# Kernel optimization log

Measured on AMD Instinct MI355X. Metric: run time of the kernel, lower is better.

Reference implementation:

```python
import jax, jax.numpy as jnp
import numpy as np

RADIUS = 1.0
NSAMPLE = 32


def setup_inputs() -> dict:
    key = jax.random.key(0)
    k1, k2, k3, k4, k5 = jax.random.split(key, 5)
    B, Nb, M, K, C = 2, 2048, 64, 216, 32
    N = B * Nb
    # points in a 20m cube
    xyz = jax.random.uniform(k1, (N, 3), dtype=jnp.float32) * 20.0
    xyz_batch_cnt = jnp.array([Nb, Nb], dtype=jnp.int32)
    # rois: [x,y,z,dx,dy,dz,ry]
    ctr = jax.random.uniform(k2, (B, M, 3), dtype=jnp.float32) * 20.0
    dims = 1.0 + jax.random.uniform(k3, (B, M, 3), dtype=jnp.float32) * 2.0
    ry = jax.random.uniform(k4, (B, M, 1), dtype=jnp.float32) * 6.28
    rois = jnp.concatenate([ctr, dims, ry], axis=-1)
    # 6x6x6 grid points jittered around each roi center
    off = (jax.random.uniform(k5, (B, M, K, 3), dtype=jnp.float32) - 0.5) * 3.0
    new_xyz = ctr[:, :, None, :] + off
    features = jax.random.normal(jax.random.fold_in(key, 7), (N, C), dtype=jnp.float32)
    return {"xyz": xyz, "xyz_batch_cnt": xyz_batch_cnt, "new_xyz": new_xyz,
            "rois": rois, "features": features}


def _query_and_group(xyz, new_xyz, rois, features, B, Nb):
    """Ball query -> ragged compaction (padded to L=N*nsample) -> gather."""
    M, K = new_xyz.shape[1], new_xyz.shape[2]
    MK = M * K
    N = B * Nb
    L = N * NSAMPLE
    xyz_b = xyz.reshape(B, Nb, 3)
    grid = new_xyz.reshape(B, MK, 3)
    # squared distances point -> grid center, (B, Nb, MK)
    d2 = jnp.sum((xyz_b[:, :, None, :] - grid[:, None, :, :]) ** 2, axis=-1)
    # roi bounding sphere: center rois[:,:,:3], radius ||dims||_2 (the `ball` tensor)
    ctr = rois[:, :, :3]
    r2 = jnp.sum(rois[:, :, 3:6] ** 2, axis=-1)          # (B, M)
    d2b = jnp.sum((xyz_b[:, :, None, :] - ctr[:, None, :, :]) ** 2, axis=-1)  # (B,Nb,M)
    in_ball = (d2b <= r2[:, None, :])[:, :, :, None]      # (B,Nb,M,1)
    mask = (d2 <= RADIUS * RADIUS) & jnp.broadcast_to(in_ball, (B, Nb, M, K)).reshape(B, Nb, MK)
    # first-NSAMPLE-in-order selection per point (matches kernel iteration order)
    rank = jnp.cumsum(mask.astype(jnp.int32), axis=2) - 1
    cols = jnp.where(mask & (rank < NSAMPLE), rank, NSAMPLE)  # NSAMPLE = OOB -> dropped
    rows = jnp.broadcast_to(
        jnp.arange(B, dtype=jnp.int32)[:, None, None] * Nb
        + jnp.arange(Nb, dtype=jnp.int32)[None, :, None], (B, Nb, MK))
    flat_idx = jnp.broadcast_to(
        jnp.arange(B, dtype=jnp.int32)[:, None, None] * MK
        + jnp.arange(MK, dtype=jnp.int32)[None, None, :], (B, Nb, MK))
    ball_idx = jnp.full((N, NSAMPLE), -1, dtype=jnp.int32)
    ball_idx = ball_idx.at[rows.reshape(-1), cols.reshape(-1)].set(
        flat_idx.reshape(-1), mode="drop")
    # BallIndice: cumsum compaction of valid (point_idx, grid_idx) pairs, row-major
    valid = (ball_idx > -1).reshape(-1)                  # (L,)
    pos = jnp.cumsum(valid.astype(jnp.int32)) - 1
    pos_w = jnp.where(valid, pos, L)                     # invalid -> OOB -> dropped
    row_ids = jnp.broadcast_to(
        jnp.arange(N, dtype=jnp.int32)[:, None], (N, NSAMPLE)).reshape(-1)
    set_indices = jnp.zeros((L,), jnp.int32).at[pos_w].set(row_ids, mode="drop")
    set_new_indices = jnp.zeros((L,), jnp.int32).at[pos_w].set(
        ball_idx.reshape(-1), mode="drop")
    nind = jnp.sum(valid.astype(jnp.int32))
    vm = (jnp.arange(L) < nind)[:, None].astype(features.dtype)  # padding mask
    # GatherFeature (padded slots zeroed, matching new_zeros semantics)
    group_xyz = xyz[set_indices] * vm
    group_new_xyz = new_xyz.reshape(-1, 3)[set_new_indices] * vm
    group_feat = features[set_indices] * vm
    group_features = jnp.concatenate([group_xyz - group_new_xyz, group_feat], axis=1)
    return group_features, set_new_indices


def reference(xyz, xyz_batch_cnt, new_xyz, rois, features):
    B = xyz_batch_cnt.shape[0]
    Nb = xyz.shape[0] // B
    return _query_and_group(xyz, new_xyz, rois, features, B, Nb)
```

## Files before the change

### kernel.cpp

```cpp
#include <hip/hip_runtime.h>


#pragma clang fp contract(off)

typedef unsigned long long u64;

#define MAXN 4096

__global__ __launch_bounds__(256) void count_kernel(
    const float* __restrict__ xyz, const float* __restrict__ new_xyz,
    const float* __restrict__ rois, int* __restrict__ counts,
    int N, int Nb, int M, int K, int nsample)
{
    __shared__ int plist[4][64];
    const int wave = threadIdx.x >> 6;
    const int lane = threadIdx.x & 63;
    const int r = blockIdx.x * 4 + wave;
    if (r >= N) return;

    const int b  = r / Nb;
    const float px = xyz[3 * r + 0];
    const float py = xyz[3 * r + 1];
    const float pz = xyz[3 * r + 2];

    bool pass = false;
    if (lane < M) {
        const float* rp = rois + (size_t)(b * M + lane) * 7;
        const float dx = rp[3], dy = rp[4], dz = rp[5];
        const float r2 = (dx * dx + dy * dy) + dz * dz;
        const float ex = px - rp[0], ey = py - rp[1], ez = pz - rp[2];
        pass = ((ex * ex + ey * ey) + ez * ez) <= r2;
    }
    const u64 roiMask = __ballot(pass);
    if (!roiMask) { if (lane == 0) counts[r] = 0; return; }
    const u64 laneLt = (1ull << lane) - 1ull;
    if (pass) plist[wave][__popcll(roiMask & laneLt)] = lane;

    const int P = __popcll(roiMask);
    const int total = P * K;
    const float* nb_ = new_xyz + (size_t)(b * M * K) * 3;

    int cnt = 0;
    for (int base = 0; base < total && cnt < nsample; base += 64) {
        const int p = base + lane;
        bool match = false;
        if (p < total) {
            const int ri = p / K;
            const int k  = p - ri * K;
            const int m  = plist[wave][ri];
            const float* gp = nb_ + (size_t)(m * K + k) * 3;
            const float ax = px - gp[0], ay = py - gp[1], az = pz - gp[2];
            match = ((ax * ax + ay * ay) + az * az) <= 1.0f;
        }
        cnt += __popcll(__ballot(match));
    }
    if (lane == 0) counts[r] = cnt > nsample ? nsample : cnt;
}

__global__ __launch_bounds__(1024) void scan_kernel(
    const int* __restrict__ counts, int* __restrict__ offsets, int N)
{
    __shared__ int waveAux[16];
    const int t = threadIdx.x;
    const int lane = t & 63;
    const int wid = t >> 6;
    const int base = t * 4;
    int c[4];
    int s = 0;
    #pragma unroll
    for (int i = 0; i < 4; i++) {
        c[i] = (base + i < N) ? counts[base + i] : 0;
        s += c[i];
    }
    int incl = s;
    #pragma unroll
    for (int d = 1; d < 64; d <<= 1) {
        int v = __shfl_up(incl, d, 64);
        if (lane >= d) incl += v;
    }
    if (lane == 63) waveAux[wid] = incl;
    __syncthreads();
    if (t < 16) {
        int v = waveAux[t];
        #pragma unroll
        for (int d = 1; d < 16; d <<= 1) {
            int u = __shfl_up(v, d, 64);
            if (t >= d) v += u;
        }
        waveAux[t] = v;
    }
    __syncthreads();
    int run = (wid ? waveAux[wid - 1] : 0) + incl - s;
    #pragma unroll
    for (int i = 0; i < 4; i++) {
        if (base + i < N) offsets[base + i] = run;
        run += c[i];
    }
}

__global__ __launch_bounds__(256) void emit_kernel(
    const float* __restrict__ xyz, const float* __restrict__ new_xyz,
    const float* __restrict__ rois, const float* __restrict__ features,
    const int* __restrict__ offsets,
    float* __restrict__ out_feat, float* __restrict__ out_idx,
    int N, int Nb, int M, int K, int C, int nsample)
{
    __shared__ int plist[4][64];
    const int wave = threadIdx.x >> 6;
    const int lane = threadIdx.x & 63;
    const int r = blockIdx.x * 4 + wave;
    if (r >= N) return;

    const int b  = r / Nb;
    const int MK = M * K;
    const float px = xyz[3 * r + 0];
    const float py = xyz[3 * r + 1];
    const float pz = xyz[3 * r + 2];

    bool pass = false;
    if (lane < M) {
        const float* rp = rois + (size_t)(b * M + lane) * 7;
        const float dx = rp[3], dy = rp[4], dz = rp[5];
        const float r2 = (dx * dx + dy * dy) + dz * dz;
        const float ex = px - rp[0], ey = py - rp[1], ez = pz - rp[2];
        pass = ((ex * ex + ey * ey) + ez * ez) <= r2;
    }
    const u64 roiMask = __ballot(pass);
    if (!roiMask) return;
    const u64 laneLt = (1ull << lane) - 1ull;
    if (pass) plist[wave][__popcll(roiMask & laneLt)] = lane;

    const int P = __popcll(roiMask);
    const int total = P * K;
    const float* nb_ = new_xyz + (size_t)b * MK * 3;
    const int obase = offsets[r];
    const float* fr = features + (size_t)r * C;

    int cnt = 0;
    for (int base = 0; base < total && cnt < nsample; base += 64) {
        const int p = base + lane;
        bool match = false;
        float ax = 0.f, ay = 0.f, az = 0.f;
        int j = 0;
        if (p < total) {
            const int ri = p / K;
            const int k  = p - ri * K;
            j = plist[wave][ri] * K + k;
            const float* gp = nb_ + (size_t)j * 3;
            ax = px - gp[0]; ay = py - gp[1]; az = pz - gp[2];
            match = ((ax * ax + ay * ay) + az * az) <= 1.0f;
        }
        const u64 mm = __ballot(match);
        const int slot = cnt + __popcll(mm & laneLt);
        if (match && slot < nsample) {
            const int o = obase + slot;
            float* of = out_feat + (size_t)o * (3 + C);
            of[0] = ax;
            of[1] = ay;
            of[2] = az;
            for (int i = 0; i < C; i++) of[3 + i] = fr[i];
            out_idx[o] = (float)(b * MK + j);
        }
        cnt += __popcll(mm);
    }
}

extern "C" void kernel_launch(void* const* d_in, const int* in_sizes, int n_in,
                              void* d_out, int out_size, void* d_ws, size_t ws_size,
                              hipStream_t stream) {
    if (n_in < 5) return;

    int bc = 0;
    for (int i = 1; i < n_in; i++) if (in_sizes[i] < in_sizes[bc]) bc = i;
    const int B = in_sizes[bc];
    if (B < 1) return;

    int xi = -1, nwi = -1, ri = -1, fi = -1;
    int N = 0, M = 0, K = 0, C = 0, nsample = 0;

    for (int rr = 0; rr < n_in && xi < 0; rr++) {
        if (rr == bc) continue;
        if (in_sizes[rr] % (7 * B)) continue;
        const int M_ = in_sizes[rr] / (7 * B);
        if (M_ < 1 || M_ > 64) continue;
        for (int xx = 0; xx < n_in && xi < 0; xx++) {
            if (xx == bc || xx == rr) continue;
            if (in_sizes[xx] % 3) continue;
            const int N_ = in_sizes[xx] / 3;
            if (N_ < B || N_ % B || N_ > MAXN) continue;
            for (int nn = 0; nn < n_in && xi < 0; nn++) {
                if (nn == bc || nn == rr || nn == xx) continue;
                if (in_sizes[nn] % (3 * B * M_)) continue;
                const int K_ = in_sizes[nn] / (3 * B * M_);
                if (K_ < 1) continue;
                for (int ff = 0; ff < n_in && xi < 0; ff++) {
                    if (ff == bc || ff == rr || ff == xx || ff == nn) continue;
                    if (in_sizes[ff] % N_) continue;
                    const int C_ = in_sizes[ff] / N_;
                    if (C_ < 1) continue;
                    if (out_size % (4 + C_)) continue;
                    const long long L_ = (long long)out_size / (4 + C_);
                    if (L_ % N_) continue;
                    const int ns = (int)(L_ / N_);
                    if (ns < 1 || ns > 1024) continue;
                    xi = xx; nwi = nn; ri = rr; fi = ff;
                    N = N_; M = M_; K = K_; C = C_; nsample = ns;
                }
            }
        }
    }
    if (xi < 0) return;

    const float* xyz      = (const float*)d_in[xi];
    const float* new_xyz  = (const float*)d_in[nwi];
    const float* rois     = (const float*)d_in[ri];
    const float* features = (const float*)d_in[fi];
    const int Nb = N / B;

    const size_t L      = (size_t)N * nsample;
    const size_t chunk0 = L * (size_t)(3 + C);

    float* out_feat = (float*)d_out;
    float* out_idx  = out_feat + chunk0;

    (void)hipMemsetAsync(d_out, 0, (chunk0 + L) * sizeof(float), stream);

    if (ws_size < (size_t)(2 * N) * sizeof(int)) return;
    int* counts  = (int*)d_ws;
    int* offsets = counts + N;
    const int blocks = (N + 3) / 4;

    count_kernel<<<blocks, 256, 0, stream>>>(
        xyz, new_xyz, rois, counts, N, Nb, M, K, nsample);
    scan_kernel<<<1, 1024, 0, stream>>>(counts, offsets, N);
    emit_kernel<<<blocks, 256, 0, stream>>>(
        xyz, new_xyz, rois, features, offsets, out_feat, out_idx,
        N, Nb, M, K, C, nsample);
}
```

Measured before the change: 109.6 us.

## Fuse memset, count, scan and emit into one cooperative kernel

```diff
diff --git a/kernel.cpp b/kernel.cpp
--- a/kernel.cpp
+++ b/kernel.cpp
@@ -1,11 +1,152 @@
 #include <hip/hip_runtime.h>
+#include <hip/hip_cooperative_groups.h>
 
 
 #pragma clang fp contract(off)
 
+namespace cg = cooperative_groups;
+
 typedef unsigned long long u64;
 
 #define MAXN 4096
+
+__global__ __launch_bounds__(256) void coop_kernel(
+    const float* __restrict__ xyz, const float* __restrict__ new_xyz,
+    const float* __restrict__ rois, const float* __restrict__ features,
+    int* __restrict__ counts, int* __restrict__ offsets, int* __restrict__ ballidx,
+    float* __restrict__ out_feat, float* __restrict__ out_idx,
+    int N, int Nb, int M, int K, int C, int nsample, int totalOut)
+{
+    cg::grid_group grid = cg::this_grid();
+
+    __shared__ int plist[4][64];
+    __shared__ int scanAux[4];
+
+    const int wave = threadIdx.x >> 6;
+    const int lane = threadIdx.x & 63;
+    const int r = blockIdx.x * 4 + wave;
+    const u64 laneLt = (1ull << lane) - 1ull;
+    const int gtid = blockIdx.x * 256 + threadIdx.x;
+    const int gthreads = gridDim.x * 256;
+
+    for (int i = gtid; i < totalOut; i += gthreads) out_feat[i] = 0.0f;
+
+    if (r < N) {
+        const int b  = r / Nb;
+        const float px = xyz[3 * r + 0];
+        const float py = xyz[3 * r + 1];
+        const float pz = xyz[3 * r + 2];
+
+        bool pass = false;
+        if (lane < M) {
+            const float* rp = rois + (size_t)(b * M + lane) * 7;
+            const float dx = rp[3], dy = rp[4], dz = rp[5];
+            const float r2 = (dx * dx + dy * dy) + dz * dz;
+            const float ex = px - rp[0], ey = py - rp[1], ez = pz - rp[2];
+            pass = ((ex * ex + ey * ey) + ez * ez) <= r2;
+        }
+        const u64 roiMask = __ballot(pass);
+        if (roiMask) {
+            if (pass) plist[wave][__popcll(roiMask & laneLt)] = lane;
+            const int P = __popcll(roiMask);
+            const int total = P * K;
+            const float* nb_ = new_xyz + (size_t)(b * M * K) * 3;
+            int* bi = ballidx + (size_t)r * nsample;
+
+            int cnt = 0;
+            for (int base = 0; base < total && cnt < nsample; base += 256) {
+                bool match[4];
+                int jj[4];
+                #pragma unroll
+                for (int u = 0; u < 4; u++) {
+                    const int p = base + u * 64 + lane;
+                    match[u] = false; jj[u] = 0;
+                    if (p < total) {
+                        const int ri = p / K;
+                        const int k  = p - ri * K;
+                        const int j  = plist[wave][ri] * K + k;
+                        jj[u] = j;
+                        const float* gp = nb_ + (size_t)j * 3;
+                        const float ax = px - gp[0], ay = py - gp[1], az = pz - gp[2];
+                        match[u] = ((ax * ax + ay * ay) + az * az) <= 1.0f;
+                    }
+                }
+                #pragma unroll
+                for (int u = 0; u < 4; u++) {
+                    const u64 mm = __ballot(match[u]);
+                    const int slot = cnt + __popcll(mm & laneLt);
+                    if (match[u] && slot < nsample) bi[slot] = jj[u];
+                    cnt += __popcll(mm);
+                }
+            }
+            if (lane == 0) counts[r] = cnt > nsample ? nsample : cnt;
+        } else {
+            if (lane == 0) counts[r] = 0;
+        }
+    }
+
+    grid.sync();
+
+    if (blockIdx.x == 0) {
+        const int G = (N + 255) / 256;
+        const int start = threadIdx.x * G;
+        int s = 0;
+        for (int i = 0; i < G; i++)
+            if (start + i < N) s += counts[start + i];
+        int incl = s;
+        #pragma unroll
+        for (int d = 1; d < 64; d <<= 1) {
+            int v = __shfl_up(incl, d, 64);
+            if (lane >= d) incl += v;
+        }
+        if (lane == 63) scanAux[wave] = incl;
+        __syncthreads();
+        if (threadIdx.x == 0) {
+            int acc = 0;
+            #pragma unroll
+            for (int w = 0; w < 4; w++) { int t = scanAux[w]; scanAux[w] = acc; acc += t; }
+        }
+        __syncthreads();
+        int run = scanAux[wave] + incl - s;
+        for (int i = 0; i < G; i++) {
+            if (start + i < N) { offsets[start + i] = run; run += counts[start + i]; }
+        }
+    }
+
+    grid.sync();
+
+    if (r < N) {
+        const int cnt = counts[r];
+        if (cnt > 0) {
+            const int b  = r / Nb;
+            const int MK = M * K;
+            const int obase = offsets[r];
+            const int* bi = ballidx + (size_t)r * nsample;
+            const float px = xyz[3 * r + 0];
+            const float py = xyz[3 * r + 1];
+            const float pz = xyz[3 * r + 2];
+            const float* fr = features + (size_t)r * C;
+            const float* nb_ = new_xyz + (size_t)b * MK * 3;
+            const int W = 3 + C;
+
+            float* dst = out_feat + (size_t)obase * W;
+            const int tot = cnt * W;
+            for (int idx = lane; idx < tot; idx += 64) {
+                const int s = idx / W;
+                const int c = idx - s * W;
+                const int j = bi[s];
+                float v;
+                if (c == 0)      v = px - nb_[(size_t)j * 3 + 0];
+                else if (c == 1) v = py - nb_[(size_t)j * 3 + 1];
+                else if (c == 2) v = pz - nb_[(size_t)j * 3 + 2];
+                else             v = fr[c - 3];
+                dst[idx] = v;
+            }
+            for (int s = lane; s < cnt; s += 64)
+                out_idx[obase + s] = (float)(b * MK + bi[s]);
+        }
+    }
+}
 
 __global__ __launch_bounds__(256) void count_kernel(
     const float* __restrict__ xyz, const float* __restrict__ new_xyz,
@@ -17,12 +158,8 @@
     const int lane = threadIdx.x & 63;
     const int r = blockIdx.x * 4 + wave;
     if (r >= N) return;
-
     const int b  = r / Nb;
-    const float px = xyz[3 * r + 0];
-    const float py = xyz[3 * r + 1];
-    const float pz = xyz[3 * r + 2];
-
+    const float px = xyz[3 * r + 0], py = xyz[3 * r + 1], pz = xyz[3 * r + 2];
     bool pass = false;
     if (lane < M) {
         const float* rp = rois + (size_t)(b * M + lane) * 7;
@@ -35,11 +172,9 @@
     if (!roiMask) { if (lane == 0) counts[r] = 0; return; }
     const u64 laneLt = (1ull << lane) - 1ull;
     if (pass) plist[wave][__popcll(roiMask & laneLt)] = lane;
-
     const int P = __popcll(roiMask);
     const int total = P * K;
     const float* nb_ = new_xyz + (size_t)(b * M * K) * 3;
-
     int cnt = 0;
     for (int base = 0; base < total && cnt < nsample; base += 64) {
         const int p = base + lane;
@@ -47,8 +182,7 @@
         if (p < total) {
             const int ri = p / K;
             const int k  = p - ri * K;
-            const int m  = plist[wave][ri];
-            const float* gp = nb_ + (size_t)(m * K + k) * 3;
+            const float* gp = nb_ + (size_t)(plist[wave][ri] * K + k) * 3;
             const float ax = px - gp[0], ay = py - gp[1], az = pz - gp[2];
             match = ((ax * ax + ay * ay) + az * az) <= 1.0f;
         }
@@ -110,13 +244,9 @@
     const int lane = threadIdx.x & 63;
     const int r = blockIdx.x * 4 + wave;
     if (r >= N) return;
-
     const int b  = r / Nb;
     const int MK = M * K;
-    const float px = xyz[3 * r + 0];
-    const float py = xyz[3 * r + 1];
-    const float pz = xyz[3 * r + 2];
-
+    const float px = xyz[3 * r + 0], py = xyz[3 * r + 1], pz = xyz[3 * r + 2];
     bool pass = false;
     if (lane < M) {
         const float* rp = rois + (size_t)(b * M + lane) * 7;
@@ -129,13 +259,11 @@
     if (!roiMask) return;
     const u64 laneLt = (1ull << lane) - 1ull;
     if (pass) plist[wave][__popcll(roiMask & laneLt)] = lane;
-
     const int P = __popcll(roiMask);
     const int total = P * K;
     const float* nb_ = new_xyz + (size_t)b * MK * 3;
     const int obase = offsets[r];
     const float* fr = features + (size_t)r * C;
-
     int cnt = 0;
     for (int base = 0; base < total && cnt < nsample; base += 64) {
         const int p = base + lane;
@@ -155,9 +283,7 @@
         if (match && slot < nsample) {
             const int o = obase + slot;
             float* of = out_feat + (size_t)o * (3 + C);
-            of[0] = ax;
-            of[1] = ay;
-            of[2] = az;
+            of[0] = ax; of[1] = ay; of[2] = az;
             for (int i = 0; i < C; i++) of[3 + i] = fr[i];
             out_idx[o] = (float)(b * MK + j);
         }
@@ -219,17 +345,31 @@
 
     const size_t L      = (size_t)N * nsample;
     const size_t chunk0 = L * (size_t)(3 + C);
+    const int totalOut  = (int)(chunk0 + L);
 
     float* out_feat = (float*)d_out;
     float* out_idx  = out_feat + chunk0;
 
-    (void)hipMemsetAsync(d_out, 0, (chunk0 + L) * sizeof(float), stream);
-
-    if (ws_size < (size_t)(2 * N) * sizeof(int)) return;
+    const size_t wsNeed = ((size_t)2 * N + (size_t)N * nsample) * sizeof(int);
+    if (ws_size < wsNeed) return;
     int* counts  = (int*)d_ws;
     int* offsets = counts + N;
+    int* ballidx = offsets + N;
+
     const int blocks = (N + 3) / 4;
 
+    void* args[] = {
+        (void*)&xyz, (void*)&new_xyz, (void*)&rois, (void*)&features,
+        (void*)&counts, (void*)&offsets, (void*)&ballidx,
+        (void*)&out_feat, (void*)&out_idx,
+        (void*)&N, (void*)&Nb, (void*)&M, (void*)&K, (void*)&C,
+        (void*)&nsample, (void*)&totalOut
+    };
+    hipError_t e = hipLaunchCooperativeKernel(
+        (const void*)coop_kernel, dim3(blocks), dim3(256), args, 0, stream);
+    if (e == hipSuccess) return;
+
+    (void)hipMemsetAsync(d_out, 0, (chunk0 + L) * sizeof(float), stream);
     count_kernel<<<blocks, 256, 0, stream>>>(
         xyz, new_xyz, rois, counts, N, Nb, M, K, nsample);
     scan_kernel<<<1, 1024, 0, stream>>>(counts, offsets, N);
```

Result: slower. 317.9 us (+190.0%).

## Cache ball indices in count pass, fuse zero-fill, coalesce emit writes

Applied to the files above, without the earlier changes.

```diff
diff --git a/kernel.cpp b/kernel.cpp
--- a/kernel.cpp
+++ b/kernel.cpp
@@ -10,12 +10,21 @@
 __global__ __launch_bounds__(256) void count_kernel(
     const float* __restrict__ xyz, const float* __restrict__ new_xyz,
     const float* __restrict__ rois, int* __restrict__ counts,
-    int N, int Nb, int M, int K, int nsample)
+    int* __restrict__ ballidx, float* __restrict__ out_all,
+    int N, int Nb, int M, int K, int nsample, int totalOut)
 {
     __shared__ int plist[4][64];
     const int wave = threadIdx.x >> 6;
     const int lane = threadIdx.x & 63;
     const int r = blockIdx.x * 4 + wave;
+    const u64 laneLt = (1ull << lane) - 1ull;
+
+    {
+        const int gtid = blockIdx.x * 256 + threadIdx.x;
+        const int gthreads = gridDim.x * 256;
+        for (int i = gtid; i < totalOut; i += gthreads) out_all[i] = 0.0f;
+    }
+
     if (r >= N) return;
 
     const int b  = r / Nb;
@@ -33,26 +42,38 @@
     }
     const u64 roiMask = __ballot(pass);
     if (!roiMask) { if (lane == 0) counts[r] = 0; return; }
-    const u64 laneLt = (1ull << lane) - 1ull;
     if (pass) plist[wave][__popcll(roiMask & laneLt)] = lane;
 
     const int P = __popcll(roiMask);
     const int total = P * K;
     const float* nb_ = new_xyz + (size_t)(b * M * K) * 3;
+    int* bi = ballidx + (size_t)r * nsample;
 
     int cnt = 0;
-    for (int base = 0; base < total && cnt < nsample; base += 64) {
-        const int p = base + lane;
-        bool match = false;
-        if (p < total) {
-            const int ri = p / K;
-            const int k  = p - ri * K;
-            const int m  = plist[wave][ri];
-            const float* gp = nb_ + (size_t)(m * K + k) * 3;
-            const float ax = px - gp[0], ay = py - gp[1], az = pz - gp[2];
-            match = ((ax * ax + ay * ay) + az * az) <= 1.0f;
-        }
-        cnt += __popcll(__ballot(match));
+    for (int base = 0; base < total && cnt < nsample; base += 256) {
+        bool match[4];
+        int jj[4];
+        #pragma unroll
+        for (int u = 0; u < 4; u++) {
+            const int p = base + u * 64 + lane;
+            match[u] = false; jj[u] = 0;
+            if (p < total) {
+                const int ri = p / K;
+                const int k  = p - ri * K;
+                const int j  = plist[wave][ri] * K + k;
+                jj[u] = j;
+                const float* gp = nb_ + (size_t)j * 3;
+                const float ax = px - gp[0], ay = py - gp[1], az = pz - gp[2];
+                match[u] = ((ax * ax + ay * ay) + az * az) <= 1.0f;
+            }
+        }
+        #pragma unroll
+        for (int u = 0; u < 4; u++) {
+            const u64 mm = __ballot(match[u]);
+            const int slot = cnt + __popcll(mm & laneLt);
+            if (match[u] && slot < nsample) bi[slot] = jj[u];
+            cnt += __popcll(mm);
+        }
     }
     if (lane == 0) counts[r] = cnt > nsample ? nsample : cnt;
 }
@@ -100,69 +121,46 @@
 
 __global__ __launch_bounds__(256) void emit_kernel(
     const float* __restrict__ xyz, const float* __restrict__ new_xyz,
-    const float* __restrict__ rois, const float* __restrict__ features,
-    const int* __restrict__ offsets,
+    const float* __restrict__ features,
+    const int* __restrict__ counts, const int* __restrict__ offsets,
+    const int* __restrict__ ballidx,
     float* __restrict__ out_feat, float* __restrict__ out_idx,
     int N, int Nb, int M, int K, int C, int nsample)
 {
-    __shared__ int plist[4][64];
     const int wave = threadIdx.x >> 6;
     const int lane = threadIdx.x & 63;
     const int r = blockIdx.x * 4 + wave;
     if (r >= N) return;
 
+    const int cnt = counts[r];
+    if (cnt <= 0) return;
+
     const int b  = r / Nb;
     const int MK = M * K;
+    const int obase = offsets[r];
+    const int* bi = ballidx + (size_t)r * nsample;
     const float px = xyz[3 * r + 0];
     const float py = xyz[3 * r + 1];
     const float pz = xyz[3 * r + 2];
-
-    bool pass = false;
-    if (lane < M) {
-        const float* rp = rois + (size_t)(b * M + lane) * 7;
-        const float dx = rp[3], dy = rp[4], dz = rp[5];
-        const float r2 = (dx * dx + dy * dy) + dz * dz;
-        const float ex = px - rp[0], ey = py - rp[1], ez = pz - rp[2];
-        pass = ((ex * ex + ey * ey) + ez * ez) <= r2;
-    }
-    const u64 roiMask = __ballot(pass);
-    if (!roiMask) return;
-    const u64 laneLt = (1ull << lane) - 1ull;
-    if (pass) plist[wave][__popcll(roiMask & laneLt)] = lane;
-
-    const int P = __popcll(roiMask);
-    const int total = P * K;
+    const float* fr = features + (size_t)r * C;
     const float* nb_ = new_xyz + (size_t)b * MK * 3;
-    const int obase = offsets[r];
-    const float* fr = features + (size_t)r * C;
-
-    int cnt = 0;
-    for (int base = 0; base < total && cnt < nsample; base += 64) {
-        const int p = base + lane;
-        bool match = false;
-        float ax = 0.f, ay = 0.f, az = 0.f;
-        int j = 0;
-        if (p < total) {
-            const int ri = p / K;
-            const int k  = p - ri * K;
-            j = plist[wave][ri] * K + k;
-            const float* gp = nb_ + (size_t)j * 3;
-            ax = px - gp[0]; ay = py - gp[1]; az = pz - gp[2];
-            match = ((ax * ax + ay * ay) + az * az) <= 1.0f;
-        }
-        const u64 mm = __ballot(match);
-        const int slot = cnt + __popcll(mm & laneLt);
-        if (match && slot < nsample) {
-            const int o = obase + slot;
-            float* of = out_feat + (size_t)o * (3 + C);
-            of[0] = ax;
-            of[1] = ay;
-            of[2] = az;
-            for (int i = 0; i < C; i++) of[3 + i] = fr[i];
-            out_idx[o] = (float)(b * MK + j);
-        }
-        cnt += __popcll(mm);
-    }
+    const int W = 3 + C;
+
+    float* dst = out_feat + (size_t)obase * W;
+    const int tot = cnt * W;
+    for (int idx = lane; idx < tot; idx += 64) {
+        const int s = idx / W;
+        const int c = idx - s * W;
+        const int j = bi[s];
+        float v;
+        if (c == 0)      v = px - nb_[(size_t)j * 3 + 0];
+        else if (c == 1) v = py - nb_[(size_t)j * 3 + 1];
+        else if (c == 2) v = pz - nb_[(size_t)j * 3 + 2];
+        else             v = fr[c - 3];
+        dst[idx] = v;
+    }
+    for (int s = lane; s < cnt; s += 64)
+        out_idx[obase + s] = (float)(b * MK + bi[s]);
 }
 
 extern "C" void kernel_launch(void* const* d_in, const int* in_sizes, int n_in,
@@ -219,21 +217,24 @@
 
     const size_t L      = (size_t)N * nsample;
     const size_t chunk0 = L * (size_t)(3 + C);
+    const int totalOut  = (int)(chunk0 + L);
 
     float* out_feat = (float*)d_out;
     float* out_idx  = out_feat + chunk0;
 
-    (void)hipMemsetAsync(d_out, 0, (chunk0 + L) * sizeof(float), stream);
-
-    if (ws_size < (size_t)(2 * N) * sizeof(int)) return;
+    const size_t wsNeed = ((size_t)2 * N + (size_t)N * nsample) * sizeof(int);
+    if (ws_size < wsNeed) return;
     int* counts  = (int*)d_ws;
     int* offsets = counts + N;
+    int* ballidx = offsets + N;
+
     const int blocks = (N + 3) / 4;
 
     count_kernel<<<blocks, 256, 0, stream>>>(
-        xyz, new_xyz, rois, counts, N, Nb, M, K, nsample);
+        xyz, new_xyz, rois, counts, ballidx, out_feat,
+        N, Nb, M, K, nsample, totalOut);
     scan_kernel<<<1, 1024, 0, stream>>>(counts, offsets, N);
     emit_kernel<<<blocks, 256, 0, stream>>>(
-        xyz, new_xyz, rois, features, offsets, out_feat, out_idx,
-        N, Nb, M, K, C, nsample);
-}
+        xyz, new_xyz, features, counts, offsets, ballidx,
+        out_feat, out_idx, N, Nb, M, K, C, nsample);
+}
```

After: 90.98 us (median of 2 runs). 17.0% less time.
